# Optimization experiments

Hardware: AMD Instinct MI355X
Metric: run time of the kernel (lower is better)

Reference implementation:

```python
import jax, jax.numpy as jnp
import numpy as np

B, T, I, H, O = 256, 512, 64, 256, 1

def setup_inputs() -> dict:
    key = jax.random.key(0)
    ks = jax.random.split(key, 7)
    s_ih = 1.0 / np.sqrt(H)
    return {
        "x": jax.random.normal(ks[0], (B, T, I), dtype=jnp.float32),
        "W_ih": jax.random.uniform(ks[1], (H, I), jnp.float32, -s_ih, s_ih),
        "W_hh": jax.random.uniform(ks[2], (H, H), jnp.float32, -s_ih, s_ih),
        "b_ih": jax.random.uniform(ks[3], (H,), jnp.float32, -s_ih, s_ih),
        "b_hh": jax.random.uniform(ks[4], (H,), jnp.float32, -s_ih, s_ih),
        "fc_W": jax.random.uniform(ks[5], (O, H), jnp.float32, -s_ih, s_ih),
        "fc_b": jax.random.uniform(ks[6], (O,), jnp.float32, -s_ih, s_ih),
    }

def reference(x, W_ih, W_hh, b_ih, b_hh, fc_W, fc_b):
    # PyTorch RNN (tanh): h_t = tanh(x_t W_ih^T + b_ih + h_{t-1} W_hh^T + b_hh)
    # Precompute the input projection for all timesteps in one GEMM: [B,T,H]
    xW = jnp.einsum('bti,hi->bth', x, W_ih) + (b_ih + b_hh)
    xW_t = jnp.transpose(xW, (1, 0, 2))  # time-major [T,B,H] for scan
    h0 = jnp.zeros((x.shape[0], W_hh.shape[0]), dtype=x.dtype)

    def step(h, xw_t):
        h_new = jnp.tanh(xw_t + h @ W_hh.T)
        return h_new, None

    h_last, _ = jax.lax.scan(step, h0, xW_t)
    return h_last @ fc_W.T + fc_b  # [B,O]
```

## Files before the change

kernel.cpp:

```cpp
#include <hip/hip_runtime.h>
#include <stdint.h>


#define RNN_B 256
#define RNN_T 512
#define RNN_I 64
#define RNN_H 256

#define STEP(RD, WR) \
  "ds_read_b128 v[0:3], "   RD " offset:0\n\t" \
  "ds_read_b128 v[4:7], "   RD " offset:16\n\t" \
  "ds_read_b128 v[8:11], "  RD " offset:32\n\t" \
  "ds_read_b128 v[12:15], " RD " offset:48\n\t" \
  "ds_read_b128 v[16:19], " RD " offset:64\n\t" \
  "ds_read_b128 v[20:23], " RD " offset:80\n\t" \
  "ds_read_b128 v[24:27], " RD " offset:96\n\t" \
  "ds_read_b128 v[28:31], " RD " offset:112\n\t" \
  "ds_read_b128 v[32:35], v55 offset:0\n\t" \
  "ds_read_b128 v[48:51], v55 offset:16\n\t" \
  "v_add_u32 v55, 0x110, v55\n\t" \
  "s_waitcnt lgkmcnt(9)\n\t" \
  "v_pk_mul_f32 v[36:37], v[0:1], v[64:65]\n\t" \
  "v_pk_mul_f32 v[38:39], v[0:1], v[96:97]\n\t" \
  "v_pk_mul_f32 v[40:41], v[0:1], v[128:129]\n\t" \
  "v_pk_mul_f32 v[42:43], v[0:1], v[160:161]\n\t" \
  "v_pk_fma_f32 v[36:37], v[2:3], v[66:67], v[36:37]\n\t" \
  "v_pk_fma_f32 v[38:39], v[2:3], v[98:99], v[38:39]\n\t" \
  "v_pk_fma_f32 v[40:41], v[2:3], v[130:131], v[40:41]\n\t" \
  "v_pk_fma_f32 v[42:43], v[2:3], v[162:163], v[42:43]\n\t" \
  "s_waitcnt lgkmcnt(8)\n\t" \
  "v_pk_fma_f32 v[36:37], v[4:5], v[68:69], v[36:37]\n\t" \
  "v_pk_fma_f32 v[38:39], v[4:5], v[100:101], v[38:39]\n\t" \
  "v_pk_fma_f32 v[40:41], v[4:5], v[132:133], v[40:41]\n\t" \
  "v_pk_fma_f32 v[42:43], v[4:5], v[164:165], v[42:43]\n\t" \
  "v_pk_fma_f32 v[36:37], v[6:7], v[70:71], v[36:37]\n\t" \
  "v_pk_fma_f32 v[38:39], v[6:7], v[102:103], v[38:39]\n\t" \
  "v_pk_fma_f32 v[40:41], v[6:7], v[134:135], v[40:41]\n\t" \
  "v_pk_fma_f32 v[42:43], v[6:7], v[166:167], v[42:43]\n\t" \
  "s_waitcnt lgkmcnt(7)\n\t" \
  "v_pk_fma_f32 v[36:37], v[8:9], v[72:73], v[36:37]\n\t" \
  "v_pk_fma_f32 v[38:39], v[8:9], v[104:105], v[38:39]\n\t" \
  "v_pk_fma_f32 v[40:41], v[8:9], v[136:137], v[40:41]\n\t" \
  "v_pk_fma_f32 v[42:43], v[8:9], v[168:169], v[42:43]\n\t" \
  "v_pk_fma_f32 v[36:37], v[10:11], v[74:75], v[36:37]\n\t" \
  "v_pk_fma_f32 v[38:39], v[10:11], v[106:107], v[38:39]\n\t" \
  "v_pk_fma_f32 v[40:41], v[10:11], v[138:139], v[40:41]\n\t" \
  "v_pk_fma_f32 v[42:43], v[10:11], v[170:171], v[42:43]\n\t" \
  "s_waitcnt lgkmcnt(6)\n\t" \
  "v_pk_fma_f32 v[36:37], v[12:13], v[76:77], v[36:37]\n\t" \
  "v_pk_fma_f32 v[38:39], v[12:13], v[108:109], v[38:39]\n\t" \
  "v_pk_fma_f32 v[40:41], v[12:13], v[140:141], v[40:41]\n\t" \
  "v_pk_fma_f32 v[42:43], v[12:13], v[172:173], v[42:43]\n\t" \
  "v_pk_fma_f32 v[36:37], v[14:15], v[78:79], v[36:37]\n\t" \
  "v_pk_fma_f32 v[38:39], v[14:15], v[110:111], v[38:39]\n\t" \
  "v_pk_fma_f32 v[40:41], v[14:15], v[142:143], v[40:41]\n\t" \
  "v_pk_fma_f32 v[42:43], v[14:15], v[174:175], v[42:43]\n\t" \
  "s_waitcnt lgkmcnt(5)\n\t" \
  "v_pk_fma_f32 v[36:37], v[16:17], v[80:81], v[36:37]\n\t" \
  "v_pk_fma_f32 v[38:39], v[16:17], v[112:113], v[38:39]\n\t" \
  "v_pk_fma_f32 v[40:41], v[16:17], v[144:145], v[40:41]\n\t" \
  "v_pk_fma_f32 v[42:43], v[16:17], v[176:177], v[42:43]\n\t" \
  "v_pk_fma_f32 v[36:37], v[18:19], v[82:83], v[36:37]\n\t" \
  "v_pk_fma_f32 v[38:39], v[18:19], v[114:115], v[38:39]\n\t" \
  "v_pk_fma_f32 v[40:41], v[18:19], v[146:147], v[40:41]\n\t" \
  "v_pk_fma_f32 v[42:43], v[18:19], v[178:179], v[42:43]\n\t" \
  "s_waitcnt lgkmcnt(4)\n\t" \
  "v_pk_fma_f32 v[36:37], v[20:21], v[84:85], v[36:37]\n\t" \
  "v_pk_fma_f32 v[38:39], v[20:21], v[116:117], v[38:39]\n\t" \
  "v_pk_fma_f32 v[40:41], v[20:21], v[148:149], v[40:41]\n\t" \
  "v_pk_fma_f32 v[42:43], v[20:21], v[180:181], v[42:43]\n\t" \
  "v_pk_fma_f32 v[36:37], v[22:23], v[86:87], v[36:37]\n\t" \
  "v_pk_fma_f32 v[38:39], v[22:23], v[118:119], v[38:39]\n\t" \
  "v_pk_fma_f32 v[40:41], v[22:23], v[150:151], v[40:41]\n\t" \
  "v_pk_fma_f32 v[42:43], v[22:23], v[182:183], v[42:43]\n\t" \
  "s_waitcnt lgkmcnt(3)\n\t" \
  "v_pk_fma_f32 v[36:37], v[24:25], v[88:89], v[36:37]\n\t" \
  "v_pk_fma_f32 v[38:39], v[24:25], v[120:121], v[38:39]\n\t" \
  "v_pk_fma_f32 v[40:41], v[24:25], v[152:153], v[40:41]\n\t" \
  "v_pk_fma_f32 v[42:43], v[24:25], v[184:185], v[42:43]\n\t" \
  "v_pk_fma_f32 v[36:37], v[26:27], v[90:91], v[36:37]\n\t" \
  "v_pk_fma_f32 v[38:39], v[26:27], v[122:123], v[38:39]\n\t" \
  "v_pk_fma_f32 v[40:41], v[26:27], v[154:155], v[40:41]\n\t" \
  "v_pk_fma_f32 v[42:43], v[26:27], v[186:187], v[42:43]\n\t" \
  "s_waitcnt lgkmcnt(2)\n\t" \
  "v_pk_fma_f32 v[36:37], v[28:29], v[92:93], v[36:37]\n\t" \
  "v_pk_fma_f32 v[38:39], v[28:29], v[124:125], v[38:39]\n\t" \
  "v_pk_fma_f32 v[40:41], v[28:29], v[156:157], v[40:41]\n\t" \
  "v_pk_fma_f32 v[42:43], v[28:29], v[188:189], v[42:43]\n\t" \
  "v_pk_fma_f32 v[36:37], v[30:31], v[94:95], v[36:37]\n\t" \
  "v_pk_fma_f32 v[38:39], v[30:31], v[126:127], v[38:39]\n\t" \
  "v_pk_fma_f32 v[40:41], v[30:31], v[158:159], v[40:41]\n\t" \
  "v_pk_fma_f32 v[42:43], v[30:31], v[190:191], v[42:43]\n\t" \
  "s_waitcnt lgkmcnt(1)\n\t" \
  "v_pk_fma_f32 v[36:37], v[32:33], v[192:193], v[36:37]\n\t" \
  "v_pk_fma_f32 v[38:39], v[32:33], v[200:201], v[38:39]\n\t" \
  "v_pk_fma_f32 v[40:41], v[32:33], v[208:209], v[40:41]\n\t" \
  "v_pk_fma_f32 v[42:43], v[32:33], v[216:217], v[42:43]\n\t" \
  "v_pk_fma_f32 v[36:37], v[34:35], v[194:195], v[36:37]\n\t" \
  "v_pk_fma_f32 v[38:39], v[34:35], v[202:203], v[38:39]\n\t" \
  "v_pk_fma_f32 v[40:41], v[34:35], v[210:211], v[40:41]\n\t" \
  "v_pk_fma_f32 v[42:43], v[34:35], v[218:219], v[42:43]\n\t" \
  "s_waitcnt lgkmcnt(0)\n\t" \
  "v_pk_fma_f32 v[36:37], v[48:49], v[196:197], v[36:37]\n\t" \
  "v_pk_fma_f32 v[38:39], v[48:49], v[204:205], v[38:39]\n\t" \
  "v_pk_fma_f32 v[40:41], v[48:49], v[212:213], v[40:41]\n\t" \
  "v_pk_fma_f32 v[42:43], v[48:49], v[220:221], v[42:43]\n\t" \
  "v_pk_fma_f32 v[36:37], v[50:51], v[198:199], v[36:37]\n\t" \
  "v_pk_fma_f32 v[38:39], v[50:51], v[206:207], v[38:39]\n\t" \
  "v_pk_fma_f32 v[40:41], v[50:51], v[214:215], v[40:41]\n\t" \
  "v_pk_fma_f32 v[42:43], v[50:51], v[222:223], v[42:43]\n\t" \
  "v_add_f32 v44, v36, v37\n\t" \
  "v_add_f32 v45, v38, v39\n\t" \
  "v_add_f32 v46, v40, v41\n\t" \
  "v_add_f32 v47, v42, v43\n\t" \
   \
  "v_cndmask_b32 v52, v46, v44, %[m1]\n\t" \
  "v_cndmask_b32 v44, v44, v46, %[m1]\n\t" \
  "v_cndmask_b32 v53, v47, v45, %[m1]\n\t" \
  "v_cndmask_b32 v45, v45, v47, %[m1]\n\t" \
  "s_nop 1\n\t" \
  "v_mov_b32_dpp v52, v52 quad_perm:[1,0,3,2] row_mask:0xf bank_mask:0xf\n\t" \
  "v_mov_b32_dpp v53, v53 quad_perm:[1,0,3,2] row_mask:0xf bank_mask:0xf\n\t" \
  "v_add_f32 v44, v44, v52\n\t" \
  "v_add_f32 v45, v45, v53\n\t" \
   \
  "v_cndmask_b32 v52, v45, v44, %[m2]\n\t" \
  "v_cndmask_b32 v44, v44, v45, %[m2]\n\t" \
  "s_nop 1\n\t" \
  "v_mov_b32_dpp v52, v52 quad_perm:[2,3,0,1] row_mask:0xf bank_mask:0xf\n\t" \
  "v_add_f32 v44, v44, v52\n\t" \
   \
  "ds_swizzle_b32 v52, v44 offset:0x101F\n\t" \
  "s_waitcnt lgkmcnt(0)\n\t" \
  "v_add_f32 v44, v44, v52\n\t" \
  "v_add_f32 v44, %[bias], v44\n\t" \
  "v_max_f32 v44, %[klo], v44\n\t" \
  "v_min_f32 v44, %[khi], v44\n\t" \
  "v_mul_f32 v44, %[km], v44\n\t" \
  "v_exp_f32 v53, v44\n\t" \
  "s_nop 1\n\t" \
  "v_subrev_f32 v54, 1.0, v53\n\t" \
  "v_add_f32 v53, 1.0, v53\n\t" \
  "v_rcp_f32 v53, v53\n\t" \
  "s_nop 1\n\t" \
  "v_mul_f32 v54, v54, v53\n\t" \
  "v_mov_b32 %[hj], v54\n\t" \
  "ds_write_b32 " WR ", v54\n\t" \
  "s_waitcnt lgkmcnt(0)\n\t" \
  "s_barrier\n\t"

__global__
__attribute__((amdgpu_flat_work_group_size(512, 512), amdgpu_waves_per_eu(2, 2)))
void rnn_fused_kernel(const float* __restrict__ x,
                      const float* __restrict__ W_ih,
                      const float* __restrict__ W_hh,
                      const float* __restrict__ b_ih,
                      const float* __restrict__ b_hh,
                      const float* __restrict__ fc_W,
                      const float* __restrict__ fc_b,
                      float* __restrict__ out)
{
    const int b   = blockIdx.x;
    const int tid = threadIdx.x;
    const int w   = tid >> 6;
    const int l   = tid & 63;
    const int g   = l >> 3;
    const int s   = l & 7;
    const int j0  = w * 32 + g * 4;

    __shared__ float hbuf[2][320];
    __shared__ float xt[32 * 68];
    __shared__ float red[8];

    const int   jjsel = ((s & 1) << 1) | ((s >> 1) & 1);
    const int   j_fin = j0 + jjsel;
    const int   jslot = j_fin + 4 * w;
    const int   wslot = (s < 4) ? jslot : (288 + (l & 31));
    const float bias2 = b_ih[j_fin] + b_hh[j_fin];
    const float fcw   = fc_W[j_fin];

    const uint32_t hb   = (uint32_t)(uintptr_t)&hbuf[0][0];
    const uint32_t xtb  = (uint32_t)(uintptr_t)&xt[0];
    const uint32_t hrd0 = hb + 144u * (uint32_t)s;
    const uint32_t hrd1 = hb + 1280u + 144u * (uint32_t)s;
    const uint32_t hwr0 = hb + 4u * (uint32_t)wslot;
    const uint32_t hwr1 = hb + 1280u + 4u * (uint32_t)wslot;
    const uint32_t xst  = xtb + 272u * (uint32_t)(tid >> 4)
                              + 16u * (uint32_t)(tid & 15)
                              + 16u * (uint32_t)((tid & 15) >> 3);
    const uint32_t xrd0 = xtb + 32u * (uint32_t)s + 16u * (uint32_t)(s >> 2);

    const unsigned long long m1 = __ballot(s & 1);
    const unsigned long long m2 = __ballot(s & 2);

    const float* whp = W_hh + (size_t)j0 * RNN_H + 32 * s;
    const float* wip = W_ih + (size_t)j0 * RNN_I + 8 * s;
    const float* xgp = x + (size_t)b * RNN_T * RNN_I + 4 * tid;
    const uint32_t whlo = (uint32_t)(uintptr_t)whp, whhi = (uint32_t)((uintptr_t)whp >> 32);
    const uint32_t wilo = (uint32_t)(uintptr_t)wip, wihi = (uint32_t)((uintptr_t)wip >> 32);
    const uint32_t xglo = (uint32_t)(uintptr_t)xgp, xghi = (uint32_t)((uintptr_t)xgp >> 32);

    if (tid < 320) hbuf[0][tid] = 0.0f;
    __syncthreads();

    float hj = 0.0f;
    int cntt, cnts, sadv;
    const float khi = 10.0f, klo = -10.0f, km = 2.8853900817779268f;

    asm volatile(
        "v_mov_b32 v56, %[whlo]\n\t"
        "v_mov_b32 v57, %[whhi]\n\t"
        "global_load_dwordx4 v[64:67],   v[56:57], off\n\t"
        "global_load_dwordx4 v[68:71],   v[56:57], off offset:16\n\t"
        "global_load_dwordx4 v[72:75],   v[56:57], off offset:32\n\t"
        "global_load_dwordx4 v[76:79],   v[56:57], off offset:48\n\t"
        "global_load_dwordx4 v[80:83],   v[56:57], off offset:64\n\t"
        "global_load_dwordx4 v[84:87],   v[56:57], off offset:80\n\t"
        "global_load_dwordx4 v[88:91],   v[56:57], off offset:96\n\t"
        "global_load_dwordx4 v[92:95],   v[56:57], off offset:112\n\t"
        "global_load_dwordx4 v[96:99],   v[56:57], off offset:1024\n\t"
        "global_load_dwordx4 v[100:103], v[56:57], off offset:1040\n\t"
        "global_load_dwordx4 v[104:107], v[56:57], off offset:1056\n\t"
        "global_load_dwordx4 v[108:111], v[56:57], off offset:1072\n\t"
        "global_load_dwordx4 v[112:115], v[56:57], off offset:1088\n\t"
        "global_load_dwordx4 v[116:119], v[56:57], off offset:1104\n\t"
        "global_load_dwordx4 v[120:123], v[56:57], off offset:1120\n\t"
        "global_load_dwordx4 v[124:127], v[56:57], off offset:1136\n\t"
        "global_load_dwordx4 v[128:131], v[56:57], off offset:2048\n\t"
        "global_load_dwordx4 v[132:135], v[56:57], off offset:2064\n\t"
        "global_load_dwordx4 v[136:139], v[56:57], off offset:2080\n\t"
        "global_load_dwordx4 v[140:143], v[56:57], off offset:2096\n\t"
        "global_load_dwordx4 v[144:147], v[56:57], off offset:2112\n\t"
        "global_load_dwordx4 v[148:151], v[56:57], off offset:2128\n\t"
        "global_load_dwordx4 v[152:155], v[56:57], off offset:2144\n\t"
        "global_load_dwordx4 v[156:159], v[56:57], off offset:2160\n\t"
        "global_load_dwordx4 v[160:163], v[56:57], off offset:3072\n\t"
        "global_load_dwordx4 v[164:167], v[56:57], off offset:3088\n\t"
        "global_load_dwordx4 v[168:171], v[56:57], off offset:3104\n\t"
        "global_load_dwordx4 v[172:175], v[56:57], off offset:3120\n\t"
        "global_load_dwordx4 v[176:179], v[56:57], off offset:3136\n\t"
        "global_load_dwordx4 v[180:183], v[56:57], off offset:3152\n\t"
        "global_load_dwordx4 v[184:187], v[56:57], off offset:3168\n\t"
        "global_load_dwordx4 v[188:191], v[56:57], off offset:3184\n\t"
        "v_mov_b32 v56, %[wilo]\n\t"
        "v_mov_b32 v57, %[wihi]\n\t"
        "global_load_dwordx4 v[192:195], v[56:57], off\n\t"
        "global_load_dwordx4 v[196:199], v[56:57], off offset:16\n\t"
        "global_load_dwordx4 v[200:203], v[56:57], off offset:256\n\t"
        "global_load_dwordx4 v[204:207], v[56:57], off offset:272\n\t"
        "global_load_dwordx4 v[208:211], v[56:57], off offset:512\n\t"
        "global_load_dwordx4 v[212:215], v[56:57], off offset:528\n\t"
        "global_load_dwordx4 v[216:219], v[56:57], off offset:768\n\t"
        "global_load_dwordx4 v[220:223], v[56:57], off offset:784\n\t"
        "v_mov_b32 v58, %[xglo]\n\t"
        "v_mov_b32 v59, %[xghi]\n\t"
        "global_load_dwordx4 v[60:63], v[58:59], off\n\t"
        "v_add_co_u32 v58, vcc, 0x2000, v58\n\t"
        "v_addc_co_u32 v59, vcc, 0, v59, vcc\n\t"
        "s_mov_b32 %[cntt], 16\n\t"
        "LTILE%=:\n\t"
        "s_waitcnt vmcnt(0)\n\t"
        "ds_write_b128 %[xst], v[60:63]\n\t"
        "global_load_dwordx4 v[60:63], v[58:59], off\n\t"
        "s_cmp_lg_u32 %[cntt], 2\n\t"
        "s_cselect_b32 %[sadv], 0x2000, 0\n\t"
        "v_add_co_u32 v58, vcc, %[sadv], v58\n\t"
        "v_addc_co_u32 v59, vcc, 0, v59, vcc\n\t"
        "v_mov_b32 v55, %[xrd0]\n\t"
        "s_waitcnt lgkmcnt(0)\n\t"
        "s_barrier\n\t"
        "s_mov_b32 %[cnts], 16\n\t"
        "LSTEP%=:\n\t"
        STEP("%[hrd0]", "%[hwr1]")
        STEP("%[hrd1]", "%[hwr0]")
        "s_sub_u32 %[cnts], %[cnts], 1\n\t"
        "s_cmp_lg_u32 %[cnts], 0\n\t"
        "s_cbranch_scc1 LSTEP%=\n\t"
        "s_sub_u32 %[cntt], %[cntt], 1\n\t"
        "s_cmp_lg_u32 %[cntt], 0\n\t"
        "s_cbranch_scc1 LTILE%=\n\t"
        "s_waitcnt vmcnt(0)\n\t"
        : [hj] "+v"(hj), [cntt] "=&s"(cntt), [cnts] "=&s"(cnts), [sadv] "=&s"(sadv)
        : [whlo] "v"(whlo), [whhi] "v"(whhi), [wilo] "v"(wilo), [wihi] "v"(wihi),
          [xglo] "v"(xglo), [xghi] "v"(xghi), [xst] "v"(xst), [xrd0] "v"(xrd0),
          [hrd0] "v"(hrd0), [hrd1] "v"(hrd1), [hwr0] "v"(hwr0), [hwr1] "v"(hwr1),
          [bias] "v"(bias2),
          [m1] "s"(m1), [m2] "s"(m2),
          [khi] "s"(khi), [klo] "s"(klo), [km] "s"(km)
        : "memory", "vcc", "scc",
          "v0","v1","v2","v3","v4","v5","v6","v7","v8","v9",
          "v10","v11","v12","v13","v14","v15","v16","v17","v18","v19",
          "v20","v21","v22","v23","v24","v25","v26","v27","v28","v29",
          "v30","v31","v32","v33","v34","v35","v36","v37","v38","v39",
          "v40","v41","v42","v43","v44","v45","v46","v47","v48","v49",
          "v50","v51","v52","v53","v54","v55","v56","v57","v58","v59",
          "v60","v61","v62","v63","v64","v65","v66","v67","v68","v69",
          "v70","v71","v72","v73","v74","v75","v76","v77","v78","v79",
          "v80","v81","v82","v83","v84","v85","v86","v87","v88","v89",
          "v90","v91","v92","v93","v94","v95","v96","v97","v98","v99",
          "v100","v101","v102","v103","v104","v105","v106","v107","v108","v109",
          "v110","v111","v112","v113","v114","v115","v116","v117","v118","v119",
          "v120","v121","v122","v123","v124","v125","v126","v127","v128","v129",
          "v130","v131","v132","v133","v134","v135","v136","v137","v138","v139",
          "v140","v141","v142","v143","v144","v145","v146","v147","v148","v149",
          "v150","v151","v152","v153","v154","v155","v156","v157","v158","v159",
          "v160","v161","v162","v163","v164","v165","v166","v167","v168","v169",
          "v170","v171","v172","v173","v174","v175","v176","v177","v178","v179",
          "v180","v181","v182","v183","v184","v185","v186","v187","v188","v189",
          "v190","v191","v192","v193","v194","v195","v196","v197","v198","v199",
          "v200","v201","v202","v203","v204","v205","v206","v207","v208","v209",
          "v210","v211","v212","v213","v214","v215","v216","v217","v218","v219",
          "v220","v221","v222","v223");

    float term = (s < 4) ? hj * fcw : 0.0f;
    #pragma unroll
    for (int d = 1; d < 64; d <<= 1) term += __shfl_xor(term, d, 64);
    if (l == 0) red[w] = term;
    __syncthreads();
    if (tid == 0) {
        float sum = 0.f;
        #pragma unroll
        for (int ww = 0; ww < 8; ++ww) sum += red[ww];
        out[b] = sum + fc_b[0];
    }
}

extern "C" void kernel_launch(void* const* d_in, const int* in_sizes, int n_in,
                              void* d_out, int out_size, void* d_ws, size_t ws_size,
                              hipStream_t stream) {
    const float* x    = (const float*)d_in[0];
    const float* W_ih = (const float*)d_in[1];
    const float* W_hh = (const float*)d_in[2];
    const float* b_ih = (const float*)d_in[3];
    const float* b_hh = (const float*)d_in[4];
    const float* fc_W = (const float*)d_in[5];
    const float* fc_b = (const float*)d_in[6];
    float* out = (float*)d_out;

    rnn_fused_kernel<<<RNN_B, 512, 0, stream>>>(x, W_ih, W_hh, b_ih, b_hh, fc_W, fc_b, out);
}
```

Baseline: 321.6 us.

## Repartition RNN step: 8 outputs per lane group over 16-way K split

Result: slower. 338.3 us (+5.2%).

```diff
diff --git a/kernel.cpp b/kernel.cpp
--- a/kernel.cpp
+++ b/kernel.cpp
@@ -12,132 +12,146 @@
   "ds_read_b128 v[4:7], "   RD " offset:16\n\t" \
   "ds_read_b128 v[8:11], "  RD " offset:32\n\t" \
   "ds_read_b128 v[12:15], " RD " offset:48\n\t" \
-  "ds_read_b128 v[16:19], " RD " offset:64\n\t" \
-  "ds_read_b128 v[20:23], " RD " offset:80\n\t" \
-  "ds_read_b128 v[24:27], " RD " offset:96\n\t" \
-  "ds_read_b128 v[28:31], " RD " offset:112\n\t" \
-  "ds_read_b128 v[32:35], v55 offset:0\n\t" \
-  "ds_read_b128 v[48:51], v55 offset:16\n\t" \
-  "v_add_u32 v55, 0x110, v55\n\t" \
-  "s_waitcnt lgkmcnt(9)\n\t" \
-  "v_pk_mul_f32 v[36:37], v[0:1], v[64:65]\n\t" \
-  "v_pk_mul_f32 v[38:39], v[0:1], v[96:97]\n\t" \
-  "v_pk_mul_f32 v[40:41], v[0:1], v[128:129]\n\t" \
-  "v_pk_mul_f32 v[42:43], v[0:1], v[160:161]\n\t" \
-  "v_pk_fma_f32 v[36:37], v[2:3], v[66:67], v[36:37]\n\t" \
-  "v_pk_fma_f32 v[38:39], v[2:3], v[98:99], v[38:39]\n\t" \
-  "v_pk_fma_f32 v[40:41], v[2:3], v[130:131], v[40:41]\n\t" \
-  "v_pk_fma_f32 v[42:43], v[2:3], v[162:163], v[42:43]\n\t" \
-  "s_waitcnt lgkmcnt(8)\n\t" \
-  "v_pk_fma_f32 v[36:37], v[4:5], v[68:69], v[36:37]\n\t" \
-  "v_pk_fma_f32 v[38:39], v[4:5], v[100:101], v[38:39]\n\t" \
-  "v_pk_fma_f32 v[40:41], v[4:5], v[132:133], v[40:41]\n\t" \
-  "v_pk_fma_f32 v[42:43], v[4:5], v[164:165], v[42:43]\n\t" \
-  "v_pk_fma_f32 v[36:37], v[6:7], v[70:71], v[36:37]\n\t" \
-  "v_pk_fma_f32 v[38:39], v[6:7], v[102:103], v[38:39]\n\t" \
-  "v_pk_fma_f32 v[40:41], v[6:7], v[134:135], v[40:41]\n\t" \
-  "v_pk_fma_f32 v[42:43], v[6:7], v[166:167], v[42:43]\n\t" \
-  "s_waitcnt lgkmcnt(7)\n\t" \
-  "v_pk_fma_f32 v[36:37], v[8:9], v[72:73], v[36:37]\n\t" \
-  "v_pk_fma_f32 v[38:39], v[8:9], v[104:105], v[38:39]\n\t" \
-  "v_pk_fma_f32 v[40:41], v[8:9], v[136:137], v[40:41]\n\t" \
-  "v_pk_fma_f32 v[42:43], v[8:9], v[168:169], v[42:43]\n\t" \
-  "v_pk_fma_f32 v[36:37], v[10:11], v[74:75], v[36:37]\n\t" \
-  "v_pk_fma_f32 v[38:39], v[10:11], v[106:107], v[38:39]\n\t" \
-  "v_pk_fma_f32 v[40:41], v[10:11], v[138:139], v[40:41]\n\t" \
-  "v_pk_fma_f32 v[42:43], v[10:11], v[170:171], v[42:43]\n\t" \
-  "s_waitcnt lgkmcnt(6)\n\t" \
-  "v_pk_fma_f32 v[36:37], v[12:13], v[76:77], v[36:37]\n\t" \
-  "v_pk_fma_f32 v[38:39], v[12:13], v[108:109], v[38:39]\n\t" \
-  "v_pk_fma_f32 v[40:41], v[12:13], v[140:141], v[40:41]\n\t" \
-  "v_pk_fma_f32 v[42:43], v[12:13], v[172:173], v[42:43]\n\t" \
-  "v_pk_fma_f32 v[36:37], v[14:15], v[78:79], v[36:37]\n\t" \
-  "v_pk_fma_f32 v[38:39], v[14:15], v[110:111], v[38:39]\n\t" \
-  "v_pk_fma_f32 v[40:41], v[14:15], v[142:143], v[40:41]\n\t" \
-  "v_pk_fma_f32 v[42:43], v[14:15], v[174:175], v[42:43]\n\t" \
-  "s_waitcnt lgkmcnt(5)\n\t" \
-  "v_pk_fma_f32 v[36:37], v[16:17], v[80:81], v[36:37]\n\t" \
-  "v_pk_fma_f32 v[38:39], v[16:17], v[112:113], v[38:39]\n\t" \
-  "v_pk_fma_f32 v[40:41], v[16:17], v[144:145], v[40:41]\n\t" \
-  "v_pk_fma_f32 v[42:43], v[16:17], v[176:177], v[42:43]\n\t" \
-  "v_pk_fma_f32 v[36:37], v[18:19], v[82:83], v[36:37]\n\t" \
-  "v_pk_fma_f32 v[38:39], v[18:19], v[114:115], v[38:39]\n\t" \
-  "v_pk_fma_f32 v[40:41], v[18:19], v[146:147], v[40:41]\n\t" \
-  "v_pk_fma_f32 v[42:43], v[18:19], v[178:179], v[42:43]\n\t" \
+  "ds_read_b128 v[16:19], v55 offset:0\n\t" \
+  "v_add_u32 v55, 0x100, v55\n\t" \
   "s_waitcnt lgkmcnt(4)\n\t" \
-  "v_pk_fma_f32 v[36:37], v[20:21], v[84:85], v[36:37]\n\t" \
-  "v_pk_fma_f32 v[38:39], v[20:21], v[116:117], v[38:39]\n\t" \
-  "v_pk_fma_f32 v[40:41], v[20:21], v[148:149], v[40:41]\n\t" \
-  "v_pk_fma_f32 v[42:43], v[20:21], v[180:181], v[42:43]\n\t" \
-  "v_pk_fma_f32 v[36:37], v[22:23], v[86:87], v[36:37]\n\t" \
-  "v_pk_fma_f32 v[38:39], v[22:23], v[118:119], v[38:39]\n\t" \
-  "v_pk_fma_f32 v[40:41], v[22:23], v[150:151], v[40:41]\n\t" \
-  "v_pk_fma_f32 v[42:43], v[22:23], v[182:183], v[42:43]\n\t" \
+  "v_pk_mul_f32 v[20:21], v[0:1], v[64:65]\n\t" \
+  "v_pk_mul_f32 v[22:23], v[0:1], v[80:81]\n\t" \
+  "v_pk_mul_f32 v[24:25], v[0:1], v[96:97]\n\t" \
+  "v_pk_mul_f32 v[26:27], v[0:1], v[112:113]\n\t" \
+  "v_pk_mul_f32 v[28:29], v[0:1], v[128:129]\n\t" \
+  "v_pk_mul_f32 v[30:31], v[0:1], v[144:145]\n\t" \
+  "v_pk_mul_f32 v[32:33], v[0:1], v[160:161]\n\t" \
+  "v_pk_mul_f32 v[34:35], v[0:1], v[176:177]\n\t" \
+  "v_pk_fma_f32 v[20:21], v[2:3], v[66:67], v[20:21]\n\t" \
+  "v_pk_fma_f32 v[22:23], v[2:3], v[82:83], v[22:23]\n\t" \
+  "v_pk_fma_f32 v[24:25], v[2:3], v[98:99], v[24:25]\n\t" \
+  "v_pk_fma_f32 v[26:27], v[2:3], v[114:115], v[26:27]\n\t" \
+  "v_pk_fma_f32 v[28:29], v[2:3], v[130:131], v[28:29]\n\t" \
+  "v_pk_fma_f32 v[30:31], v[2:3], v[146:147], v[30:31]\n\t" \
+  "v_pk_fma_f32 v[32:33], v[2:3], v[162:163], v[32:33]\n\t" \
+  "v_pk_fma_f32 v[34:35], v[2:3], v[178:179], v[34:35]\n\t" \
   "s_waitcnt lgkmcnt(3)\n\t" \
-  "v_pk_fma_f32 v[36:37], v[24:25], v[88:89], v[36:37]\n\t" \
-  "v_pk_fma_f32 v[38:39], v[24:25], v[120:121], v[38:39]\n\t" \
-  "v_pk_fma_f32 v[40:41], v[24:25], v[152:153], v[40:41]\n\t" \
-  "v_pk_fma_f32 v[42:43], v[24:25], v[184:185], v[42:43]\n\t" \
-  "v_pk_fma_f32 v[36:37], v[26:27], v[90:91], v[36:37]\n\t" \
-  "v_pk_fma_f32 v[38:39], v[26:27], v[122:123], v[38:39]\n\t" \
-  "v_pk_fma_f32 v[40:41], v[26:27], v[154:155], v[40:41]\n\t" \
-  "v_pk_fma_f32 v[42:43], v[26:27], v[186:187], v[42:43]\n\t" \
+  "v_pk_fma_f32 v[20:21], v[4:5], v[68:69], v[20:21]\n\t" \
+  "v_pk_fma_f32 v[22:23], v[4:5], v[84:85], v[22:23]\n\t" \
+  "v_pk_fma_f32 v[24:25], v[4:5], v[100:101], v[24:25]\n\t" \
+  "v_pk_fma_f32 v[26:27], v[4:5], v[116:117], v[26:27]\n\t" \
+  "v_pk_fma_f32 v[28:29], v[4:5], v[132:133], v[28:29]\n\t" \
+  "v_pk_fma_f32 v[30:31], v[4:5], v[148:149], v[30:31]\n\t" \
+  "v_pk_fma_f32 v[32:33], v[4:5], v[164:165], v[32:33]\n\t" \
+  "v_pk_fma_f32 v[34:35], v[4:5], v[180:181], v[34:35]\n\t" \
+  "v_pk_fma_f32 v[20:21], v[6:7], v[70:71], v[20:21]\n\t" \
+  "v_pk_fma_f32 v[22:23], v[6:7], v[86:87], v[22:23]\n\t" \
+  "v_pk_fma_f32 v[24:25], v[6:7], v[102:103], v[24:25]\n\t" \
+  "v_pk_fma_f32 v[26:27], v[6:7], v[118:119], v[26:27]\n\t" \
+  "v_pk_fma_f32 v[28:29], v[6:7], v[134:135], v[28:29]\n\t" \
+  "v_pk_fma_f32 v[30:31], v[6:7], v[150:151], v[30:31]\n\t" \
+  "v_pk_fma_f32 v[32:33], v[6:7], v[166:167], v[32:33]\n\t" \
+  "v_pk_fma_f32 v[34:35], v[6:7], v[182:183], v[34:35]\n\t" \
   "s_waitcnt lgkmcnt(2)\n\t" \
-  "v_pk_fma_f32 v[36:37], v[28:29], v[92:93], v[36:37]\n\t" \
-  "v_pk_fma_f32 v[38:39], v[28:29], v[124:125], v[38:39]\n\t" \
-  "v_pk_fma_f32 v[40:41], v[28:29], v[156:157], v[40:41]\n\t" \
-  "v_pk_fma_f32 v[42:43], v[28:29], v[188:189], v[42:43]\n\t" \
-  "v_pk_fma_f32 v[36:37], v[30:31], v[94:95], v[36:37]\n\t" \
-  "v_pk_fma_f32 v[38:39], v[30:31], v[126:127], v[38:39]\n\t" \
-  "v_pk_fma_f32 v[40:41], v[30:31], v[158:159], v[40:41]\n\t" \
-  "v_pk_fma_f32 v[42:43], v[30:31], v[190:191], v[42:43]\n\t" \
+  "v_pk_fma_f32 v[20:21], v[8:9], v[72:73], v[20:21]\n\t" \
+  "v_pk_fma_f32 v[22:23], v[8:9], v[88:89], v[22:23]\n\t" \
+  "v_pk_fma_f32 v[24:25], v[8:9], v[104:105], v[24:25]\n\t" \
+  "v_pk_fma_f32 v[26:27], v[8:9], v[120:121], v[26:27]\n\t" \
+  "v_pk_fma_f32 v[28:29], v[8:9], v[136:137], v[28:29]\n\t" \
+  "v_pk_fma_f32 v[30:31], v[8:9], v[152:153], v[30:31]\n\t" \
+  "v_pk_fma_f32 v[32:33], v[8:9], v[168:169], v[32:33]\n\t" \
+  "v_pk_fma_f32 v[34:35], v[8:9], v[184:185], v[34:35]\n\t" \
+  "v_pk_fma_f32 v[20:21], v[10:11], v[74:75], v[20:21]\n\t" \
+  "v_pk_fma_f32 v[22:23], v[10:11], v[90:91], v[22:23]\n\t" \
+  "v_pk_fma_f32 v[24:25], v[10:11], v[106:107], v[24:25]\n\t" \
+  "v_pk_fma_f32 v[26:27], v[10:11], v[122:123], v[26:27]\n\t" \
+  "v_pk_fma_f32 v[28:29], v[10:11], v[138:139], v[28:29]\n\t" \
+  "v_pk_fma_f32 v[30:31], v[10:11], v[154:155], v[30:31]\n\t" \
+  "v_pk_fma_f32 v[32:33], v[10:11], v[170:171], v[32:33]\n\t" \
+  "v_pk_fma_f32 v[34:35], v[10:11], v[186:187], v[34:35]\n\t" \
   "s_waitcnt lgkmcnt(1)\n\t" \
-  "v_pk_fma_f32 v[36:37], v[32:33], v[192:193], v[36:37]\n\t" \
-  "v_pk_fma_f32 v[38:39], v[32:33], v[200:201], v[38:39]\n\t" \
-  "v_pk_fma_f32 v[40:41], v[32:33], v[208:209], v[40:41]\n\t" \
-  "v_pk_fma_f32 v[42:43], v[32:33], v[216:217], v[42:43]\n\t" \
-  "v_pk_fma_f32 v[36:37], v[34:35], v[194:195], v[36:37]\n\t" \
-  "v_pk_fma_f32 v[38:39], v[34:35], v[202:203], v[38:39]\n\t" \
-  "v_pk_fma_f32 v[40:41], v[34:35], v[210:211], v[40:41]\n\t" \
-  "v_pk_fma_f32 v[42:43], v[34:35], v[218:219], v[42:43]\n\t" \
+  "v_pk_fma_f32 v[20:21], v[12:13], v[76:77], v[20:21]\n\t" \
+  "v_pk_fma_f32 v[22:23], v[12:13], v[92:93], v[22:23]\n\t" \
+  "v_pk_fma_f32 v[24:25], v[12:13], v[108:109], v[24:25]\n\t" \
+  "v_pk_fma_f32 v[26:27], v[12:13], v[124:125], v[26:27]\n\t" \
+  "v_pk_fma_f32 v[28:29], v[12:13], v[140:141], v[28:29]\n\t" \
+  "v_pk_fma_f32 v[30:31], v[12:13], v[156:157], v[30:31]\n\t" \
+  "v_pk_fma_f32 v[32:33], v[12:13], v[172:173], v[32:33]\n\t" \
+  "v_pk_fma_f32 v[34:35], v[12:13], v[188:189], v[34:35]\n\t" \
+  "v_pk_fma_f32 v[20:21], v[14:15], v[78:79], v[20:21]\n\t" \
+  "v_pk_fma_f32 v[22:23], v[14:15], v[94:95], v[22:23]\n\t" \
+  "v_pk_fma_f32 v[24:25], v[14:15], v[110:111], v[24:25]\n\t" \
+  "v_pk_fma_f32 v[26:27], v[14:15], v[126:127], v[26:27]\n\t" \
+  "v_pk_fma_f32 v[28:29], v[14:15], v[142:143], v[28:29]\n\t" \
+  "v_pk_fma_f32 v[30:31], v[14:15], v[158:159], v[30:31]\n\t" \
+  "v_pk_fma_f32 v[32:33], v[14:15], v[174:175], v[32:33]\n\t" \
+  "v_pk_fma_f32 v[34:35], v[14:15], v[190:191], v[34:35]\n\t" \
   "s_waitcnt lgkmcnt(0)\n\t" \
-  "v_pk_fma_f32 v[36:37], v[48:49], v[196:197], v[36:37]\n\t" \
-  "v_pk_fma_f32 v[38:39], v[48:49], v[204:205], v[38:39]\n\t" \
-  "v_pk_fma_f32 v[40:41], v[48:49], v[212:213], v[40:41]\n\t" \
-  "v_pk_fma_f32 v[42:43], v[48:49], v[220:221], v[42:43]\n\t" \
-  "v_pk_fma_f32 v[36:37], v[50:51], v[198:199], v[36:37]\n\t" \
-  "v_pk_fma_f32 v[38:39], v[50:51], v[206:207], v[38:39]\n\t" \
-  "v_pk_fma_f32 v[40:41], v[50:51], v[214:215], v[40:41]\n\t" \
-  "v_pk_fma_f32 v[42:43], v[50:51], v[222:223], v[42:43]\n\t" \
-  "v_add_f32 v44, v36, v37\n\t" \
-  "v_add_f32 v45, v38, v39\n\t" \
-  "v_add_f32 v46, v40, v41\n\t" \
-  "v_add_f32 v47, v42, v43\n\t" \
-   \
-  "v_cndmask_b32 v52, v46, v44, %[m1]\n\t" \
-  "v_cndmask_b32 v44, v44, v46, %[m1]\n\t" \
-  "v_cndmask_b32 v53, v47, v45, %[m1]\n\t" \
-  "v_cndmask_b32 v45, v45, v47, %[m1]\n\t" \
-  "s_nop 1\n\t" \
-  "v_mov_b32_dpp v52, v52 quad_perm:[1,0,3,2] row_mask:0xf bank_mask:0xf\n\t" \
-  "v_mov_b32_dpp v53, v53 quad_perm:[1,0,3,2] row_mask:0xf bank_mask:0xf\n\t" \
-  "v_add_f32 v44, v44, v52\n\t" \
-  "v_add_f32 v45, v45, v53\n\t" \
-   \
-  "v_cndmask_b32 v52, v45, v44, %[m2]\n\t" \
-  "v_cndmask_b32 v44, v44, v45, %[m2]\n\t" \
-  "s_nop 1\n\t" \
-  "v_mov_b32_dpp v52, v52 quad_perm:[2,3,0,1] row_mask:0xf bank_mask:0xf\n\t" \
-  "v_add_f32 v44, v44, v52\n\t" \
-   \
-  "ds_swizzle_b32 v52, v44 offset:0x101F\n\t" \
+  "v_pk_fma_f32 v[20:21], v[16:17], v[192:193], v[20:21]\n\t" \
+  "v_pk_fma_f32 v[22:23], v[16:17], v[196:197], v[22:23]\n\t" \
+  "v_pk_fma_f32 v[24:25], v[16:17], v[200:201], v[24:25]\n\t" \
+  "v_pk_fma_f32 v[26:27], v[16:17], v[204:205], v[26:27]\n\t" \
+  "v_pk_fma_f32 v[28:29], v[16:17], v[208:209], v[28:29]\n\t" \
+  "v_pk_fma_f32 v[30:31], v[16:17], v[212:213], v[30:31]\n\t" \
+  "v_pk_fma_f32 v[32:33], v[16:17], v[216:217], v[32:33]\n\t" \
+  "v_pk_fma_f32 v[34:35], v[16:17], v[220:221], v[34:35]\n\t" \
+  "v_pk_fma_f32 v[20:21], v[18:19], v[194:195], v[20:21]\n\t" \
+  "v_pk_fma_f32 v[22:23], v[18:19], v[198:199], v[22:23]\n\t" \
+  "v_pk_fma_f32 v[24:25], v[18:19], v[202:203], v[24:25]\n\t" \
+  "v_pk_fma_f32 v[26:27], v[18:19], v[206:207], v[26:27]\n\t" \
+  "v_pk_fma_f32 v[28:29], v[18:19], v[210:211], v[28:29]\n\t" \
+  "v_pk_fma_f32 v[30:31], v[18:19], v[214:215], v[30:31]\n\t" \
+  "v_pk_fma_f32 v[32:33], v[18:19], v[218:219], v[32:33]\n\t" \
+  "v_pk_fma_f32 v[34:35], v[18:19], v[222:223], v[34:35]\n\t" \
+   \
+  "v_add_f32 v36, v20, v21\n\t" \
+  "v_add_f32 v37, v22, v23\n\t" \
+  "v_add_f32 v38, v24, v25\n\t" \
+  "v_add_f32 v39, v26, v27\n\t" \
+  "v_add_f32 v40, v28, v29\n\t" \
+  "v_add_f32 v41, v30, v31\n\t" \
+  "v_add_f32 v42, v32, v33\n\t" \
+  "v_add_f32 v43, v34, v35\n\t" \
+   \
+  "v_cndmask_b32 v44, v37, v36, %[m1]\n\t" \
+  "v_cndmask_b32 v36, v36, v37, %[m1]\n\t" \
+  "v_cndmask_b32 v45, v39, v38, %[m1]\n\t" \
+  "v_cndmask_b32 v38, v38, v39, %[m1]\n\t" \
+  "v_cndmask_b32 v46, v41, v40, %[m1]\n\t" \
+  "v_cndmask_b32 v40, v40, v41, %[m1]\n\t" \
+  "v_cndmask_b32 v47, v43, v42, %[m1]\n\t" \
+  "v_cndmask_b32 v42, v42, v43, %[m1]\n\t" \
+  "s_nop 1\n\t" \
+  "v_mov_b32_dpp v44, v44 quad_perm:[1,0,3,2] row_mask:0xf bank_mask:0xf\n\t" \
+  "v_mov_b32_dpp v45, v45 quad_perm:[1,0,3,2] row_mask:0xf bank_mask:0xf\n\t" \
+  "v_mov_b32_dpp v46, v46 quad_perm:[1,0,3,2] row_mask:0xf bank_mask:0xf\n\t" \
+  "v_mov_b32_dpp v47, v47 quad_perm:[1,0,3,2] row_mask:0xf bank_mask:0xf\n\t" \
+  "v_add_f32 v36, v36, v44\n\t" \
+  "v_add_f32 v38, v38, v45\n\t" \
+  "v_add_f32 v40, v40, v46\n\t" \
+  "v_add_f32 v42, v42, v47\n\t" \
+   \
+  "v_cndmask_b32 v44, v38, v36, %[m2]\n\t" \
+  "v_cndmask_b32 v36, v36, v38, %[m2]\n\t" \
+  "v_cndmask_b32 v45, v42, v40, %[m2]\n\t" \
+  "v_cndmask_b32 v40, v40, v42, %[m2]\n\t" \
+  "s_nop 1\n\t" \
+  "v_mov_b32_dpp v44, v44 quad_perm:[2,3,0,1] row_mask:0xf bank_mask:0xf\n\t" \
+  "v_mov_b32_dpp v45, v45 quad_perm:[2,3,0,1] row_mask:0xf bank_mask:0xf\n\t" \
+  "v_add_f32 v36, v36, v44\n\t" \
+  "v_add_f32 v40, v40, v45\n\t" \
+   \
+  "v_cndmask_b32 v44, v40, v36, %[m4]\n\t" \
+  "v_cndmask_b32 v36, v36, v40, %[m4]\n\t" \
+  "ds_swizzle_b32 v44, v44 offset:0x101F\n\t" \
   "s_waitcnt lgkmcnt(0)\n\t" \
-  "v_add_f32 v44, v44, v52\n\t" \
-  "v_add_f32 v44, %[bias], v44\n\t" \
-  "v_max_f32 v44, %[klo], v44\n\t" \
-  "v_min_f32 v44, %[khi], v44\n\t" \
-  "v_mul_f32 v44, %[km], v44\n\t" \
-  "v_exp_f32 v53, v44\n\t" \
+  "v_add_f32 v36, v36, v44\n\t" \
+   \
+  "s_nop 1\n\t" \
+  "v_mov_b32_dpp v44, v36 row_ror:8 row_mask:0xf bank_mask:0xf\n\t" \
+  "v_add_f32 v36, v36, v44\n\t" \
+   \
+  "v_add_f32 v36, %[bias], v36\n\t" \
+  "v_max_f32 v36, %[klo], v36\n\t" \
+  "v_min_f32 v36, %[khi], v36\n\t" \
+  "v_mul_f32 v36, %[km], v36\n\t" \
+  "v_exp_f32 v53, v36\n\t" \
   "s_nop 1\n\t" \
   "v_subrev_f32 v54, 1.0, v53\n\t" \
   "v_add_f32 v53, 1.0, v53\n\t" \
@@ -164,43 +178,41 @@
     const int tid = threadIdx.x;
     const int w   = tid >> 6;
     const int l   = tid & 63;
-    const int g   = l >> 3;
-    const int s   = l & 7;
-    const int j0  = w * 32 + g * 4;
-
-    __shared__ float hbuf[2][320];
-    __shared__ float xt[32 * 68];
+    const int g   = l >> 4;
+    const int s   = l & 15;
+    const int j0  = w * 32 + g * 8;
+
+    __shared__ float hbuf[2][384];
+    __shared__ float xt[32][RNN_I];
     __shared__ float red[8];
 
-    const int   jjsel = ((s & 1) << 1) | ((s >> 1) & 1);
-    const int   j_fin = j0 + jjsel;
-    const int   jslot = j_fin + 4 * w;
-    const int   wslot = (s < 4) ? jslot : (288 + (l & 31));
+    const int   j_fin = j0 + (s & 7);
+    const int   jslot = j_fin + 4 * (j_fin >> 4);
+    const int   wslot = (s < 8) ? jslot : (320 + (l & 31));
     const float bias2 = b_ih[j_fin] + b_hh[j_fin];
     const float fcw   = fc_W[j_fin];
 
     const uint32_t hb   = (uint32_t)(uintptr_t)&hbuf[0][0];
-    const uint32_t xtb  = (uint32_t)(uintptr_t)&xt[0];
-    const uint32_t hrd0 = hb + 144u * (uint32_t)s;
-    const uint32_t hrd1 = hb + 1280u + 144u * (uint32_t)s;
+    const uint32_t xtb  = (uint32_t)(uintptr_t)&xt[0][0];
+    const uint32_t hrd0 = hb + 80u * (uint32_t)s;
+    const uint32_t hrd1 = hb + 1536u + 80u * (uint32_t)s;
     const uint32_t hwr0 = hb + 4u * (uint32_t)wslot;
-    const uint32_t hwr1 = hb + 1280u + 4u * (uint32_t)wslot;
-    const uint32_t xst  = xtb + 272u * (uint32_t)(tid >> 4)
-                              + 16u * (uint32_t)(tid & 15)
-                              + 16u * (uint32_t)((tid & 15) >> 3);
-    const uint32_t xrd0 = xtb + 32u * (uint32_t)s + 16u * (uint32_t)(s >> 2);
-
-    const unsigned long long m1 = __ballot(s & 1);
-    const unsigned long long m2 = __ballot(s & 2);
-
-    const float* whp = W_hh + (size_t)j0 * RNN_H + 32 * s;
-    const float* wip = W_ih + (size_t)j0 * RNN_I + 8 * s;
+    const uint32_t hwr1 = hb + 1536u + 4u * (uint32_t)wslot;
+    const uint32_t xst  = xtb + 256u * (uint32_t)(tid >> 4) + 16u * (uint32_t)(tid & 15);
+    const uint32_t xrd0 = xtb + 16u * (uint32_t)s;
+
+    const unsigned long long m1 = __ballot(l & 1);
+    const unsigned long long m2 = __ballot(l & 2);
+    const unsigned long long m4 = __ballot(l & 4);
+
+    const float* whp = W_hh + (size_t)j0 * RNN_H + 16 * s;
+    const float* wip = W_ih + (size_t)j0 * RNN_I + 4 * s;
     const float* xgp = x + (size_t)b * RNN_T * RNN_I + 4 * tid;
     const uint32_t whlo = (uint32_t)(uintptr_t)whp, whhi = (uint32_t)((uintptr_t)whp >> 32);
     const uint32_t wilo = (uint32_t)(uintptr_t)wip, wihi = (uint32_t)((uintptr_t)wip >> 32);
     const uint32_t xglo = (uint32_t)(uintptr_t)xgp, xghi = (uint32_t)((uintptr_t)xgp >> 32);
 
-    if (tid < 320) hbuf[0][tid] = 0.0f;
+    if (tid < 384) hbuf[0][tid] = 0.0f;
     __syncthreads();
 
     float hj = 0.0f;
@@ -210,48 +222,50 @@
     asm volatile(
         "v_mov_b32 v56, %[whlo]\n\t"
         "v_mov_b32 v57, %[whhi]\n\t"
+        "v_add_co_u32 v58, vcc, 0x1000, v56\n\t"
+        "v_addc_co_u32 v59, vcc, 0, v57, vcc\n\t"
         "global_load_dwordx4 v[64:67],   v[56:57], off\n\t"
         "global_load_dwordx4 v[68:71],   v[56:57], off offset:16\n\t"
         "global_load_dwordx4 v[72:75],   v[56:57], off offset:32\n\t"
         "global_load_dwordx4 v[76:79],   v[56:57], off offset:48\n\t"
-        "global_load_dwordx4 v[80:83],   v[56:57], off offset:64\n\t"
-        "global_load_dwordx4 v[84:87],   v[56:57], off offset:80\n\t"
-        "global_load_dwordx4 v[88:91],   v[56:57], off offset:96\n\t"
-        "global_load_dwordx4 v[92:95],   v[56:57], off offset:112\n\t"
-        "global_load_dwordx4 v[96:99],   v[56:57], off offset:1024\n\t"
-        "global_load_dwordx4 v[100:103], v[56:57], off offset:1040\n\t"
-        "global_load_dwordx4 v[104:107], v[56:57], off offset:1056\n\t"
-        "global_load_dwordx4 v[108:111], v[56:57], off offset:1072\n\t"
-        "global_load_dwordx4 v[112:115], v[56:57], off offset:1088\n\t"
-        "global_load_dwordx4 v[116:119], v[56:57], off offset:1104\n\t"
-        "global_load_dwordx4 v[120:123], v[56:57], off offset:1120\n\t"
-        "global_load_dwordx4 v[124:127], v[56:57], off offset:1136\n\t"
-        "global_load_dwordx4 v[128:131], v[56:57], off offset:2048\n\t"
-        "global_load_dwordx4 v[132:135], v[56:57], off offset:2064\n\t"
-        "global_load_dwordx4 v[136:139], v[56:57], off offset:2080\n\t"
-        "global_load_dwordx4 v[140:143], v[56:57], off offset:2096\n\t"
-        "global_load_dwordx4 v[144:147], v[56:57], off offset:2112\n\t"
-        "global_load_dwordx4 v[148:151], v[56:57], off offset:2128\n\t"
-        "global_load_dwordx4 v[152:155], v[56:57], off offset:2144\n\t"
-        "global_load_dwordx4 v[156:159], v[56:57], off offset:2160\n\t"
-        "global_load_dwordx4 v[160:163], v[56:57], off offset:3072\n\t"
-        "global_load_dwordx4 v[164:167], v[56:57], off offset:3088\n\t"
-        "global_load_dwordx4 v[168:171], v[56:57], off offset:3104\n\t"
-        "global_load_dwordx4 v[172:175], v[56:57], off offset:3120\n\t"
-        "global_load_dwordx4 v[176:179], v[56:57], off offset:3136\n\t"
-        "global_load_dwordx4 v[180:183], v[56:57], off offset:3152\n\t"
-        "global_load_dwordx4 v[184:187], v[56:57], off offset:3168\n\t"
-        "global_load_dwordx4 v[188:191], v[56:57], off offset:3184\n\t"
+        "global_load_dwordx4 v[80:83],   v[56:57], off offset:1024\n\t"
+        "global_load_dwordx4 v[84:87],   v[56:57], off offset:1040\n\t"
+        "global_load_dwordx4 v[88:91],   v[56:57], off offset:1056\n\t"
+        "global_load_dwordx4 v[92:95],   v[56:57], off offset:1072\n\t"
+        "global_load_dwordx4 v[96:99],   v[56:57], off offset:2048\n\t"
+        "global_load_dwordx4 v[100:103], v[56:57], off offset:2064\n\t"
+        "global_load_dwordx4 v[104:107], v[56:57], off offset:2080\n\t"
+        "global_load_dwordx4 v[108:111], v[56:57], off offset:2096\n\t"
+        "global_load_dwordx4 v[112:115], v[56:57], off offset:3072\n\t"
+        "global_load_dwordx4 v[116:119], v[56:57], off offset:3088\n\t"
+        "global_load_dwordx4 v[120:123], v[56:57], off offset:3104\n\t"
+        "global_load_dwordx4 v[124:127], v[56:57], off offset:3120\n\t"
+        "global_load_dwordx4 v[128:131], v[58:59], off\n\t"
+        "global_load_dwordx4 v[132:135], v[58:59], off offset:16\n\t"
+        "global_load_dwordx4 v[136:139], v[58:59], off offset:32\n\t"
+        "global_load_dwordx4 v[140:143], v[58:59], off offset:48\n\t"
+        "global_load_dwordx4 v[144:147], v[58:59], off offset:1024\n\t"
+        "global_load_dwordx4 v[148:151], v[58:59], off offset:1040\n\t"
+        "global_load_dwordx4 v[152:155], v[58:59], off offset:1056\n\t"
+        "global_load_dwordx4 v[156:159], v[58:59], off offset:1072\n\t"
+        "global_load_dwordx4 v[160:163], v[58:59], off offset:2048\n\t"
+        "global_load_dwordx4 v[164:167], v[58:59], off offset:2064\n\t"
+        "global_load_dwordx4 v[168:171], v[58:59], off offset:2080\n\t"
+        "global_load_dwordx4 v[172:175], v[58:59], off offset:2096\n\t"
+        "global_load_dwordx4 v[176:179], v[58:59], off offset:3072\n\t"
+        "global_load_dwordx4 v[180:183], v[58:59], off offset:3088\n\t"
+        "global_load_dwordx4 v[184:187], v[58:59], off offset:3104\n\t"
+        "global_load_dwordx4 v[188:191], v[58:59], off offset:3120\n\t"
         "v_mov_b32 v56, %[wilo]\n\t"
         "v_mov_b32 v57, %[wihi]\n\t"
         "global_load_dwordx4 v[192:195], v[56:57], off\n\t"
-        "global_load_dwordx4 v[196:199], v[56:57], off offset:16\n\t"
-        "global_load_dwordx4 v[200:203], v[56:57], off offset:256\n\t"
-        "global_load_dwordx4 v[204:207], v[56:57], off offset:272\n\t"
-        "global_load_dwordx4 v[208:211], v[56:57], off offset:512\n\t"
-        "global_load_dwordx4 v[212:215], v[56:57], off offset:528\n\t"
-        "global_load_dwordx4 v[216:219], v[56:57], off offset:768\n\t"
-        "global_load_dwordx4 v[220:223], v[56:57], off offset:784\n\t"
+        "global_load_dwordx4 v[196:199], v[56:57], off offset:256\n\t"
+        "global_load_dwordx4 v[200:203], v[56:57], off offset:512\n\t"
+        "global_load_dwordx4 v[204:207], v[56:57], off offset:768\n\t"
+        "global_load_dwordx4 v[208:211], v[56:57], off offset:1024\n\t"
+        "global_load_dwordx4 v[212:215], v[56:57], off offset:1280\n\t"
+        "global_load_dwordx4 v[216:219], v[56:57], off offset:1536\n\t"
+        "global_load_dwordx4 v[220:223], v[56:57], off offset:1792\n\t"
         "v_mov_b32 v58, %[xglo]\n\t"
         "v_mov_b32 v59, %[xghi]\n\t"
         "global_load_dwordx4 v[60:63], v[58:59], off\n\t"
@@ -285,7 +299,7 @@
           [xglo] "v"(xglo), [xghi] "v"(xghi), [xst] "v"(xst), [xrd0] "v"(xrd0),
           [hrd0] "v"(hrd0), [hrd1] "v"(hrd1), [hwr0] "v"(hwr0), [hwr1] "v"(hwr1),
           [bias] "v"(bias2),
-          [m1] "s"(m1), [m2] "s"(m2),
+          [m1] "s"(m1), [m2] "s"(m2), [m4] "s"(m4),
           [khi] "s"(khi), [klo] "s"(klo), [km] "s"(km)
         : "memory", "vcc", "scc",
           "v0","v1","v2","v3","v4","v5","v6","v7","v8","v9",
@@ -312,7 +326,7 @@
           "v210","v211","v212","v213","v214","v215","v216","v217","v218","v219",
           "v220","v221","v222","v223");
 
-    float term = (s < 4) ? hj * fcw : 0.0f;
+    float term = (s < 8) ? hj * fcw : 0.0f;
     #pragma unroll
     for (int d = 1; d < 64; d <<= 1) term += __shfl_xor(term, d, 64);
     if (l == 0) red[w] = term;
```
